# Kernel tuning notes

Hardware: AMD Instinct MI355X
Metric: run time of the kernel (lower is better)

Reference implementation:

```python
import jax, jax.numpy as jnp
import numpy as np
import math

PAD_IDX = 1
BOS_IDX = 2
B, S, T = 32, 128, 64
E, H, L, V = 256, 512, 2, 32000


def _lstm_cell(gates, c):
    # torch gate order: i, f, g, o
    i, f, g, o = jnp.split(gates, 4, axis=-1)
    c_new = jax.nn.sigmoid(f) * c + jax.nn.sigmoid(i) * jnp.tanh(g)
    h_new = jax.nn.sigmoid(o) * jnp.tanh(c_new)
    return h_new, c_new


def _run_lstm_layer(x_tbi, Wih, Whh, b, h0, c0):
    def step(carry, x_t):
        h, c = carry
        h2, c2 = _lstm_cell(x_t @ Wih + h @ Whh + b, c)
        return (h2, c2), h2
    (hT, cT), ys = jax.lax.scan(step, (h0, c0), x_tbi)
    return ys, hT, cT


def setup_inputs() -> dict:
    key = jax.random.key(0)
    ks = iter(jax.random.split(key, 40))
    def w(shape, s=0.05):
        return jax.random.normal(next(ks), shape, jnp.float32) * s
    inp = {
        'src_tokens': jax.random.randint(next(ks), (B, S), 0, V, dtype=jnp.int32),
        'tgt_tokens': jax.random.randint(next(ks), (B, T), 0, V, dtype=jnp.int32),
        'src_emb': w((V, E), 0.02),
        'tgt_emb': w((V, E), 0.02),
        'enc_Wih0': w((E, 4 * H)), 'enc_Whh0': w((H, 4 * H)), 'enc_b0': jnp.zeros((4 * H,), jnp.float32),
        'enc_Wih1': w((H, 4 * H)), 'enc_Whh1': w((H, 4 * H)), 'enc_b1': jnp.zeros((4 * H,), jnp.float32),
        'dec_Wih0': w((E + H, 4 * H)), 'dec_Whh0': w((H, 4 * H)), 'dec_b0': jnp.zeros((4 * H,), jnp.float32),
        'dec_Wih1': w((H, 4 * H)), 'dec_Whh1': w((H, 4 * H)), 'dec_b1': jnp.zeros((4 * H,), jnp.float32),
        'attn_W': w((2 * H, H)), 'attn_b': jnp.zeros((H,), jnp.float32),
        'v_w': w((H,)),
        'coal_w': w((L, 1), 0.5), 'coal_b': jnp.zeros((1,), jnp.float32),
        'out_W': w((2 * H + E, V)), 'out_b': jnp.zeros((V,), jnp.float32),
    }
    return inp


def reference(src_tokens, tgt_tokens, src_emb, tgt_emb,
              enc_Wih0, enc_Whh0, enc_b0, enc_Wih1, enc_Whh1, enc_b1,
              dec_Wih0, dec_Whh0, dec_b0, dec_Wih1, dec_Whh1, dec_b1,
              attn_W, attn_b, v_w, coal_w, coal_b, out_W, out_b):
    Bq = src_tokens.shape[0]
    sqrtE_src = np.float32(math.sqrt(src_emb.shape[1]))
    sqrtE_tgt = np.float32(math.sqrt(tgt_emb.shape[1]))

    # ---- Encoder (2-layer LSTM, batch_first; dropout=0 eval) ----
    x = (src_emb[src_tokens] * sqrtE_src).transpose(1, 0, 2)  # (S,B,E)
    z = jnp.zeros((Bq, H), jnp.float32)
    ys0, hA, cA = _run_lstm_layer(x, enc_Wih0, enc_Whh0, enc_b0, z, z)
    ys1, hB, cB = _run_lstm_layer(ys0, enc_Wih1, enc_Whh1, enc_b1, z, z)
    enc_out = ys1.transpose(1, 0, 2)          # (B,S,H)
    hidden = jnp.stack([hA, hB])              # (L,B,H)
    cell = jnp.stack([cA, cB])

    mask = src_tokens != PAD_IDX              # (B,S)
    Wq, We = attn_W[:H], attn_W[H:]
    enc_proj = enc_out @ We                   # (B,S,H) loop-invariant part of attn linear

    def dec_step(carry, tok):
        h, c = carry                          # (L,B,H) each
        emb = jax.nn.relu(tgt_emb[tok] * sqrtE_tgt)          # (B,E)
        # faithful raw reshape (L,B,H) -> (B,H,L), coalesce layers
        q = jax.nn.relu(h.reshape(Bq, H, L) @ coal_w + coal_b)[..., 0]  # (B,H)
        e = jnp.tanh(enc_proj + (q @ Wq + attn_b)[:, None, :])          # (B,S,H)
        score = e @ v_w                                                 # (B,S)
        score = jnp.where(mask, score, np.float32(-1e10))
        a = jax.nn.softmax(score, axis=1)
        wctx = jnp.einsum('bs,bsh->bh', a, enc_out)                     # (B,H)
        xin = jnp.concatenate([emb, wctx], axis=-1)                     # (B,E+H)
        h0n, c0n = _lstm_cell(xin @ dec_Wih0 + h[0] @ dec_Whh0 + dec_b0, c[0])
        h1n, c1n = _lstm_cell(h0n @ dec_Wih1 + h[1] @ dec_Whh1 + dec_b1, c[1])
        logits = jnp.concatenate([h1n, wctx, emb], axis=-1) @ out_W + out_b  # (B,V)
        return (jnp.stack([h0n, h1n]), jnp.stack([c0n, c1n])), logits

    (hF, cF), outs = jax.lax.scan(dec_step, (hidden, cell), tgt_tokens[:, :-1].T)
    first = jnp.full((Bq, 1, out_b.shape[0]), np.float32(BOS_IDX))  # decoder_outputs[:,0]=BOS_IDX
    dec_outputs = jnp.concatenate([first, outs.transpose(1, 0, 2)], axis=1)  # (B,T,V)
    return dec_outputs, hF, cF
```

## Files before the change

### kernel.cpp

```cpp
#include <hip/hip_runtime.h>
#include <hip/hip_bf16.h>

typedef __bf16 bf16x8 __attribute__((ext_vector_type(8)));
typedef float f32x4 __attribute__((ext_vector_type(4)));

#define DEV static __device__ __forceinline__

constexpr int Bq = 32, Sq = 128, Tq = 64, Eq = 256, Hq = 512, Vq = 32000;
constexpr int G4 = 2048;
constexpr int TD = 63;
constexpr int KOUT = 1280;
constexpr float SQRTE = 16.0f;

DEV float sigf(float x) { return 1.0f / (1.0f + __expf(-x)); }
DEV float tanh_fast(float x) {
    float ax = fabsf(x);
    float t = __expf(-2.f * ax);
    float r = (1.f - t) / (1.f + t);
    return x < 0.f ? -r : r;
}

__global__ __launch_bounds__(256) void k_embed_src(const int* __restrict__ tok,
                                                   const float* __restrict__ emb,
                                                   __hip_bfloat16* __restrict__ x)
{
    int idx = blockIdx.x * 256 + threadIdx.x;
    int e = idx & (Eq - 1);
    int r = idx >> 8;
    int b = r & 31, t = r >> 5;
    x[idx] = __float2bfloat16(emb[(size_t)tok[b * Sq + t] * Eq + e] * SQRTE);
}

__global__ __launch_bounds__(256) void k_embed_tgt(const int* __restrict__ tok,
                                                   const float* __restrict__ emb,
                                                   __hip_bfloat16* __restrict__ embt,
                                                   __hip_bfloat16* __restrict__ Xout)
{
    int idx = blockIdx.x * 256 + threadIdx.x;
    int e = idx & (Eq - 1);
    int r = idx >> 8;
    int b = r & 31, t = r >> 5;
    float v = fmaxf(0.f, emb[(size_t)tok[b * Tq + t] * Eq + e] * SQRTE);
    embt[idx] = __float2bfloat16(v);
    Xout[(size_t)r * KOUT + 1024 + e] = __float2bfloat16(v);
}

__global__ __launch_bounds__(256) void k_transpose_bf16(const float* __restrict__ W,
                                                        __hip_bfloat16* __restrict__ Wt,
                                                        int K, int N)
{
    __shared__ float tile[32][33];
    int nb = blockIdx.x * 32, kb = blockIdx.y * 32;
    int c = threadIdx.x & 31, r4 = threadIdx.x >> 5;
    for (int i = 0; i < 32; i += 8)
        tile[r4 + i][c] = W[(size_t)(kb + r4 + i) * N + nb + c];
    __syncthreads();
    for (int i = 0; i < 32; i += 8) {
        int rr = r4 + i;
        Wt[(size_t)(nb + rr) * K + kb + c] = __float2bfloat16(tile[c][rr]);
    }
}

DEV void stage_A(const __hip_bfloat16* A, __bf16* As) {
    int tx = threadIdx.x;
#pragma unroll
    for (int p = 0; p < 8; ++p) {
        int c = tx + p * 256;
        int row = c >> 6, kc = c & 63;
        uint4 v = *(const uint4*)((const unsigned short*)A + row * 512 + kc * 8);
        int kd = kc ^ (row & 7);
        *(uint4*)(As + row * 512 + kd * 8) = v;
    }
}

DEV void mfma_pass(const __bf16* As, const unsigned short* BT, int colB,
                   int kg, int fr, f32x4* acc) {
    const unsigned short* bp = BT + (size_t)colB * 512 + kg * 8;
    int f7 = fr & 7;
#pragma unroll
    for (int k0 = 0; k0 < 512; k0 += 32) {
        int cidx = ((k0 >> 3) | kg) ^ f7;
        bf16x8 bfv = *(const bf16x8*)(bp + k0);
        bf16x8 af0 = *(const bf16x8*)(As + fr * 512 + cidx * 8);
        bf16x8 af1 = *(const bf16x8*)(As + (16 + fr) * 512 + cidx * 8);
        acc[0] = __builtin_amdgcn_mfma_f32_16x16x32_bf16(af0, bfv, acc[0], 0, 0, 0);
        acc[1] = __builtin_amdgcn_mfma_f32_16x16x32_bf16(af1, bfv, acc[1], 0, 0, 0);
    }
}

DEV void rec_core(const __hip_bfloat16* A0, const __hip_bfloat16* B0T,
                  const __hip_bfloat16* A1, const __hip_bfloat16* B1T,
                  const __hip_bfloat16* xpart, const float* bias,
                  float* cbuf, float* hf, __hip_bfloat16* hb,
                  float* ef32, int ef32_stride,
                  __hip_bfloat16* ebf16, int ebf16_stride,
                  int j0, __bf16* As0, __bf16* As1)
{
    stage_A(A0, As0);
    if (A1) stage_A(A1, As1);
    __syncthreads();

    int tx = threadIdx.x, w = tx >> 6, lane = tx & 63;
    int fr = lane & 15, kg = lane >> 4;
    int colB = w * 512 + j0 + fr;

    f32x4 acc[2];
    acc[0] = (f32x4){0.f, 0.f, 0.f, 0.f};
    acc[1] = (f32x4){0.f, 0.f, 0.f, 0.f};
    mfma_pass(As0, (const unsigned short*)B0T, colB, kg, fr, acc);
    if (B1T) mfma_pass(As1, (const unsigned short*)B1T, colB, kg, fr, acc);

    __syncthreads();
    float* gbuf = (float*)As0;
    float* gw = gbuf + w * 512;
#pragma unroll
    for (int m = 0; m < 2; ++m)
#pragma unroll
        for (int q = 0; q < 4; ++q)
            gw[(m * 16 + kg * 4 + q) * 16 + fr] = acc[m][q];
    __syncthreads();

    int idx = tx;
#pragma unroll
    for (int r = 0; r < 2; ++r, idx += 256) {
        int b = idx >> 4, jj = idx & 15, j = j0 + jj;
        float gi = gbuf[0 * 512 + b * 16 + jj];
        float gf = gbuf[1 * 512 + b * 16 + jj];
        float gg = gbuf[2 * 512 + b * 16 + jj];
        float go = gbuf[3 * 512 + b * 16 + jj];
        if (xpart) {
            gi += __bfloat162float(xpart[b * 2048 + j]);
            gf += __bfloat162float(xpart[b * 2048 + 512 + j]);
            gg += __bfloat162float(xpart[b * 2048 + 1024 + j]);
            go += __bfloat162float(xpart[b * 2048 + 1536 + j]);
        }
        if (bias) {
            gi += bias[j]; gf += bias[512 + j];
            gg += bias[1024 + j]; go += bias[1536 + j];
        }
        int ci = b * 512 + j;
        float cc = cbuf[ci];
        float cn = sigf(gf) * cc + sigf(gi) * tanh_fast(gg);
        cbuf[ci] = cn;
        float ho = sigf(go) * tanh_fast(cn);
        hf[ci] = ho;
        hb[ci] = __float2bfloat16(ho);
        if (ef32)  ef32[b * ef32_stride + j] = ho;
        if (ebf16) ebf16[b * ebf16_stride + j] = __float2bfloat16(ho);
    }
}

__global__ __launch_bounds__(256) void k_rec(
    const __hip_bfloat16* __restrict__ A0, const __hip_bfloat16* __restrict__ B0T,
    const __hip_bfloat16* __restrict__ A1, const __hip_bfloat16* __restrict__ B1T,
    const __hip_bfloat16* __restrict__ xpart, const float* __restrict__ bias,
    float* __restrict__ cbuf, float* __restrict__ hf, __hip_bfloat16* __restrict__ hb,
    __hip_bfloat16* __restrict__ ebf16, int ebf16_stride)
{
    __shared__ __align__(16) __bf16 As0[32 * 512];
    __shared__ __align__(16) __bf16 As1[32 * 512];
    rec_core(A0, B0T, A1, B1T, xpart, bias, cbuf, hf, hb,
             nullptr, 0, ebf16, ebf16_stride, blockIdx.x * 16, As0, As1);
}

__global__ __launch_bounds__(256) void k_enc2(int t,
    const __hip_bfloat16* __restrict__ X0b,
    const __hip_bfloat16* __restrict__ eWhh0T, const __hip_bfloat16* __restrict__ eWih1T,
    const __hip_bfloat16* __restrict__ eWhh1T, const float* __restrict__ eb1,
    __hip_bfloat16* __restrict__ h0b, __hip_bfloat16* __restrict__ h1b,
    float* __restrict__ h0f, float* __restrict__ h1f,
    float* __restrict__ c0, float* __restrict__ c1,
    __hip_bfloat16* __restrict__ ys0b,
    float* __restrict__ encf, __hip_bfloat16* __restrict__ encb)
{
    __shared__ __align__(16) __bf16 As0[32 * 512];
    __shared__ __align__(16) __bf16 As1[32 * 512];
    bool lay1 = blockIdx.x >= 32;
    int j0 = (blockIdx.x & 31) * 16;
    if (!lay1) {
        if (t >= 128) return;
        rec_core(h0b + (t & 1) * 16384, eWhh0T, nullptr, nullptr,
                 X0b + (size_t)t * 32 * 2048, nullptr,
                 c0, h0f, h0b + ((t + 1) & 1) * 16384,
                 nullptr, 0, ys0b + (size_t)t * 16384, 512, j0, As0, As1);
    } else {
        if (t < 1) return;
        int s = t - 1;
        rec_core(ys0b + (size_t)s * 16384, eWih1T,
                 h1b + (s & 1) * 16384, eWhh1T,
                 nullptr, eb1,
                 c1, h1f, h1b + ((s + 1) & 1) * 16384,
                 encf + s * 512, 128 * 512, encb + s * 512, 128 * 512, j0, As0, As1);
    }
}

__global__ __launch_bounds__(256) void k_attnq(
    const float* __restrict__ h0f, const float* __restrict__ h1f,
    const __hip_bfloat16* __restrict__ WqT, const float* __restrict__ attn_b,
    const float* __restrict__ coal_w, const float* __restrict__ coal_b,
    float* __restrict__ aq)
{
    __shared__ __align__(16) __bf16 Qs[32 * 512];
    int tx = threadIdx.x;
    float cw0 = coal_w[0], cw1 = coal_w[1], cb = coal_b[0];
    for (int idx = tx; idx < 16384; idx += 256) {
        int b = idx >> 9, j = idx & 511;
        int p = b * 1024 + 2 * j;
        float v0 = (p < 16384) ? h0f[p] : h1f[p - 16384];
        float v1 = (p + 1 < 16384) ? h0f[p + 1] : h1f[p + 1 - 16384];
        float q = fmaxf(0.f, v0 * cw0 + v1 * cw1 + cb);
        int kc = j >> 3, kd = kc ^ (b & 7);
        Qs[b * 512 + kd * 8 + (j & 7)] = __float2bfloat16(q);
    }
    __syncthreads();
    int w = tx >> 6, lane = tx & 63, fr = lane & 15, kg = lane >> 4;
    int col = blockIdx.x * 64 + w * 16 + fr;
    f32x4 acc[2];
    acc[0] = (f32x4){0.f, 0.f, 0.f, 0.f};
    acc[1] = (f32x4){0.f, 0.f, 0.f, 0.f};
    mfma_pass(Qs, (const unsigned short*)WqT, col, kg, fr, acc);
    float ab = attn_b[col];
#pragma unroll
    for (int m = 0; m < 2; ++m)
#pragma unroll
        for (int q = 0; q < 4; ++q)
            aq[(m * 16 + kg * 4 + q) * 512 + col] = acc[m][q] + ab;
}

__global__ __launch_bounds__(256) void k_attnsc(
    const float* __restrict__ aq, const float* __restrict__ v_w,
    const int* __restrict__ src_tok,
    const float* __restrict__ enc_proj, const float* __restrict__ enc_outf,
    __hip_bfloat16* __restrict__ wctxb, __hip_bfloat16* __restrict__ XoutT)
{
    __shared__ float aqs[512];
    __shared__ float vws[512];
    __shared__ float sc[128];
    int b = blockIdx.x;
    int tx = threadIdx.x;
    for (int i = tx; i < 512; i += 256) { aqs[i] = aq[b * 512 + i]; vws[i] = v_w[i]; }
    __syncthreads();

    int s = tx >> 1, half = tx & 1;
    const float* ep = enc_proj + ((size_t)(b * 128 + s)) * 512 + half * 256;
    float a0 = 0.f, a1 = 0.f, a2 = 0.f, a3 = 0.f;
#pragma unroll 8
    for (int ii = 0; ii < 256; ii += 4) {
        float4 f = *(const float4*)(ep + ii);
        int ib = half * 256 + ii;
        a0 += tanh_fast(f.x + aqs[ib])     * vws[ib];
        a1 += tanh_fast(f.y + aqs[ib + 1]) * vws[ib + 1];
        a2 += tanh_fast(f.z + aqs[ib + 2]) * vws[ib + 2];
        a3 += tanh_fast(f.w + aqs[ib + 3]) * vws[ib + 3];
    }
    float p = (a0 + a1) + (a2 + a3);
    p += __shfl_xor(p, 1, 64);
    if (half == 0) sc[s] = (src_tok[b * 128 + s] != 1) ? p : -1e10f;
    __syncthreads();

    if (tx < 64) {
        float m1 = fmaxf(sc[tx], sc[tx + 64]);
#pragma unroll
        for (int o = 32; o > 0; o >>= 1) m1 = fmaxf(m1, __shfl_down(m1, o, 64));
        m1 = __shfl(m1, 0, 64);
        float e0 = __expf(sc[tx] - m1), e1 = __expf(sc[tx + 64] - m1);
        float ss = e0 + e1;
#pragma unroll
        for (int o = 32; o > 0; o >>= 1) ss += __shfl_down(ss, o, 64);
        ss = __shfl(ss, 0, 64);
        float inv = 1.0f / ss;
        sc[tx] = e0 * inv; sc[tx + 64] = e1 * inv;
    }
    __syncthreads();

#pragma unroll
    for (int rr = 0; rr < 2; ++rr) {
        int i = tx + rr * 256;
        const float* eo = enc_outf + (size_t)b * 65536 + i;
        float w0 = 0.f, w1 = 0.f, w2 = 0.f, w3 = 0.f;
#pragma unroll 8
        for (int s2 = 0; s2 < 128; s2 += 4) {
            w0 += sc[s2]     * eo[(s2)     * 512];
            w1 += sc[s2 + 1] * eo[(s2 + 1) * 512];
            w2 += sc[s2 + 2] * eo[(s2 + 2) * 512];
            w3 += sc[s2 + 3] * eo[(s2 + 3) * 512];
        }
        float wv = (w0 + w1) + (w2 + w3);
        wctxb[b * 512 + i] = __float2bfloat16(wv);
        XoutT[(size_t)b * KOUT + 512 + i] = __float2bfloat16(wv);
    }
}

__global__ __launch_bounds__(256) void k_mfma(
    const __hip_bfloat16* __restrict__ A, const __hip_bfloat16* __restrict__ BT,
    const float* __restrict__ bias, float* __restrict__ Cf,
    __hip_bfloat16* __restrict__ Cb, int M, int N, int K)
{
    __shared__ __bf16 As[128][72];
    __shared__ __bf16 Bs[128][72];
    const unsigned short* Aw = (const unsigned short*)A;
    const unsigned short* Bw = (const unsigned short*)BT;
    int n0 = blockIdx.x * 128, m0 = blockIdx.y * 128;
    int tx = threadIdx.x;
    int w = tx >> 6, lane = tx & 63;
    int wm = (w >> 1) * 64, wn = (w & 1) * 64;
    int fr = lane & 15, kg = lane >> 4;
    f32x4 acc[4][4];
#pragma unroll
    for (int mi = 0; mi < 4; mi++)
#pragma unroll
        for (int ni = 0; ni < 4; ni++) acc[mi][ni] = (f32x4){0.f, 0.f, 0.f, 0.f};

    for (int k0 = 0; k0 < K; k0 += 64) {
        __syncthreads();
#pragma unroll
        for (int p = 0; p < 4; p++) {
            int ch = tx + p * 256;
            int r = ch >> 3, cc = (ch & 7) * 8;
            uint4 va = {0u, 0u, 0u, 0u};
            int m = m0 + r;
            if (m < M) va = *(const uint4*)(Aw + (size_t)m * K + k0 + cc);
            *(uint4*)(&As[r][cc]) = va;
            uint4 vb = *(const uint4*)(Bw + (size_t)(n0 + r) * K + k0 + cc);
            *(uint4*)(&Bs[r][cc]) = vb;
        }
        __syncthreads();
#pragma unroll
        for (int kk = 0; kk < 64; kk += 32) {
            bf16x8 af[4], bfv[4];
#pragma unroll
            for (int i = 0; i < 4; i++) {
                af[i]  = *(const bf16x8*)(&As[wm + i * 16 + fr][kk + kg * 8]);
                bfv[i] = *(const bf16x8*)(&Bs[wn + i * 16 + fr][kk + kg * 8]);
            }
#pragma unroll
            for (int mi = 0; mi < 4; mi++)
#pragma unroll
                for (int ni = 0; ni < 4; ni++)
                    acc[mi][ni] = __builtin_amdgcn_mfma_f32_16x16x32_bf16(
                        af[mi], bfv[ni], acc[mi][ni], 0, 0, 0);
        }
    }
#pragma unroll
    for (int ni = 0; ni < 4; ni++) {
        int n = n0 + wn + ni * 16 + fr;
        float bv = bias ? bias[n] : 0.f;
#pragma unroll
        for (int mi = 0; mi < 4; mi++) {
#pragma unroll
            for (int qd = 0; qd < 4; qd++) {
                int R = m0 + wm + mi * 16 + kg * 4 + qd;
                if (R < M) {
                    float v = acc[mi][ni][qd] + bv;
                    if (Cf) Cf[(size_t)R * N + n] = v;
                    else    Cb[(size_t)R * N + n] = __float2bfloat16(v);
                }
            }
        }
    }
}

__global__ __launch_bounds__(256) void k_init_dec(
    const float* __restrict__ h0e, const float* __restrict__ h1e,
    const float* __restrict__ c0e, const float* __restrict__ c1e,
    float* __restrict__ h0fd, float* __restrict__ h1fd,
    __hip_bfloat16* __restrict__ h0bd, __hip_bfloat16* __restrict__ h1bd,
    float* __restrict__ c0d, float* __restrict__ c1d)
{
    int idx = blockIdx.x * 256 + threadIdx.x;
    float a = h0e[idx], b = h1e[idx];
    h0fd[idx] = a; h1fd[idx] = b;
    h0bd[idx] = __float2bfloat16(a);
    h1bd[idx] = __float2bfloat16(b);
    c0d[idx] = c0e[idx];
    c1d[idx] = c1e[idx];
}

__global__ __launch_bounds__(256) void k_bos(float* __restrict__ out)
{
    int b = blockIdx.y;
    int i = blockIdx.x * 256 + threadIdx.x;
    out[(size_t)b * (Tq * Vq) + i] = 2.0f;
}

__global__ __launch_bounds__(256) void k_finalize(
    const float* __restrict__ h0f, const float* __restrict__ h1f,
    const float* __restrict__ c0f, const float* __restrict__ c1f,
    float* __restrict__ out)
{
    int idx = blockIdx.x * 256 + threadIdx.x;
    size_t base = (size_t)Bq * Tq * Vq;
    out[base + idx] = h0f[idx];
    out[base + 16384 + idx] = h1f[idx];
    out[base + 32768 + idx] = c0f[idx];
    out[base + 49152 + idx] = c1f[idx];
}

__global__ __launch_bounds__(256) void k_logits(
    const __hip_bfloat16* __restrict__ A, const __hip_bfloat16* __restrict__ Bt,
    const float* __restrict__ bias, float* __restrict__ out)
{
    __shared__ __bf16 As[128][72];
    __shared__ __bf16 Bs[128][72];
    const unsigned short* Aw = (const unsigned short*)A;
    const unsigned short* Bw = (const unsigned short*)Bt;
    int n0 = blockIdx.x * 128, m0 = blockIdx.y * 128;
    int tx = threadIdx.x;
    int w = tx >> 6, lane = tx & 63;
    int wm = (w >> 1) * 64, wn = (w & 1) * 64;
    int fr = lane & 15, kg = lane >> 4;
    f32x4 acc[4][4];
#pragma unroll
    for (int mi = 0; mi < 4; mi++)
#pragma unroll
        for (int ni = 0; ni < 4; ni++) acc[mi][ni] = (f32x4){0.f, 0.f, 0.f, 0.f};

    for (int k0 = 0; k0 < 1280; k0 += 64) {
        __syncthreads();
#pragma unroll
        for (int p = 0; p < 4; p++) {
            int ch = tx + p * 256;
            int r = ch >> 3, cc = (ch & 7) * 8;
            uint4 va = {0u, 0u, 0u, 0u};
            int m = m0 + r;
            if (m < 2016) va = *(const uint4*)(Aw + (size_t)m * 1280 + k0 + cc);
            *(uint4*)(&As[r][cc]) = va;
            uint4 vb = *(const uint4*)(Bw + (size_t)(n0 + r) * 1280 + k0 + cc);
            *(uint4*)(&Bs[r][cc]) = vb;
        }
        __syncthreads();
#pragma unroll
        for (int kk = 0; kk < 64; kk += 32) {
            bf16x8 af[4], bfv[4];
#pragma unroll
            for (int i = 0; i < 4; i++) {
                af[i]  = *(const bf16x8*)(&As[wm + i * 16 + fr][kk + kg * 8]);
                bfv[i] = *(const bf16x8*)(&Bs[wn + i * 16 + fr][kk + kg * 8]);
            }
#pragma unroll
            for (int mi = 0; mi < 4; mi++)
#pragma unroll
                for (int ni = 0; ni < 4; ni++)
                    acc[mi][ni] = __builtin_amdgcn_mfma_f32_16x16x32_bf16(
                        af[mi], bfv[ni], acc[mi][ni], 0, 0, 0);
        }
    }
#pragma unroll
    for (int ni = 0; ni < 4; ni++) {
        int n = n0 + wn + ni * 16 + fr;
        float bv = bias[n];
#pragma unroll
        for (int mi = 0; mi < 4; mi++) {
#pragma unroll
            for (int qd = 0; qd < 4; qd++) {
                int R = m0 + wm + mi * 16 + kg * 4 + qd;
                if (R < 2016) {
                    int bb = R & 31, ts = R >> 5;
                    out[(size_t)bb * (Tq * Vq) + (size_t)(ts + 1) * Vq + n] =
                        acc[mi][ni][qd] + bv;
                }
            }
        }
    }
}

extern "C" void kernel_launch(void* const* d_in, const int* in_sizes, int n_in,
                              void* d_out, int out_size, void* d_ws, size_t ws_size,
                              hipStream_t stream)
{
    (void)in_sizes; (void)n_in; (void)out_size; (void)ws_size;
    const int*   src_tok = (const int*)  d_in[0];
    const int*   tgt_tok = (const int*)  d_in[1];
    const float* src_emb = (const float*)d_in[2];
    const float* tgt_emb = (const float*)d_in[3];
    const float* eWih0   = (const float*)d_in[4];
    const float* eWhh0   = (const float*)d_in[5];
    const float* eb0     = (const float*)d_in[6];
    const float* eWih1   = (const float*)d_in[7];
    const float* eWhh1   = (const float*)d_in[8];
    const float* eb1     = (const float*)d_in[9];
    const float* dWih0   = (const float*)d_in[10];
    const float* dWhh0   = (const float*)d_in[11];
    const float* db0     = (const float*)d_in[12];
    const float* dWih1   = (const float*)d_in[13];
    const float* dWhh1   = (const float*)d_in[14];
    const float* db1     = (const float*)d_in[15];
    const float* attn_W  = (const float*)d_in[16];
    const float* attn_b  = (const float*)d_in[17];
    const float* v_w     = (const float*)d_in[18];
    const float* coal_w  = (const float*)d_in[19];
    const float* coal_b  = (const float*)d_in[20];
    const float* out_W   = (const float*)d_in[21];
    const float* out_b   = (const float*)d_in[22];
    float* out = (float*)d_out;

    char* ws = (char*)d_ws;
    size_t off = 0;
    auto alloc = [&](size_t bytes) -> char* {
        char* p = ws + off;
        off += (bytes + 255) & ~(size_t)255;
        return p;
    };
    typedef __hip_bfloat16 BF;
    BF* X0b     = (BF*)alloc(4096ull * 2048 * 2);
    BF* Xembb   = (BF*)alloc(2016ull * 2048 * 2);
    BF* x_srcb  = (BF*)alloc(4096ull * 256 * 2);
    BF* embtb   = (BF*)alloc(2016ull * 256 * 2);
    BF* ys0b    = (BF*)alloc(128ull * 16384 * 2);
    float* enc_outf = (float*)alloc(4096ull * 512 * 4);
    BF* enc_outb    = (BF*)alloc(4096ull * 512 * 2);
    float* enc_proj = (float*)alloc(4096ull * 512 * 4);
    float* aq       = (float*)alloc(16384ull * 4);
    BF* wctxb       = (BF*)alloc(16384ull * 2);
    BF* Xout        = (BF*)alloc(2016ull * 1280 * 2);
    BF* Wt          = (BF*)alloc(32000ull * 1280 * 2);
    BF* eWhh0T  = (BF*)alloc(2048ull * 512 * 2);
    BF* eWih1T  = (BF*)alloc(2048ull * 512 * 2);
    BF* eWhh1T  = (BF*)alloc(2048ull * 512 * 2);
    BF* dWih0wT = (BF*)alloc(2048ull * 512 * 2);
    BF* dWhh0T  = (BF*)alloc(2048ull * 512 * 2);
    BF* dWih1T  = (BF*)alloc(2048ull * 512 * 2);
    BF* dWhh1T  = (BF*)alloc(2048ull * 512 * 2);
    BF* eWih0T  = (BF*)alloc(2048ull * 256 * 2);
    BF* dWih0eT = (BF*)alloc(2048ull * 256 * 2);
    BF* WqT     = (BF*)alloc(512ull * 512 * 2);
    BF* WeT     = (BF*)alloc(512ull * 512 * 2);
    BF* h0b_e   = (BF*)alloc(2ull * 16384 * 2);
    BF* h1b_e   = (BF*)alloc(2ull * 16384 * 2);
    float* h0f_e = (float*)alloc(16384ull * 4);
    float* h1f_e = (float*)alloc(16384ull * 4);
    float* c0e   = (float*)alloc(16384ull * 4);
    float* c1e   = (float*)alloc(16384ull * 4);
    float* h0fd  = (float*)alloc(2ull * 16384 * 4);
    float* h1fd  = (float*)alloc(2ull * 16384 * 4);
    BF* h0bd     = (BF*)alloc(2ull * 16384 * 2);
    BF* h1bd     = (BF*)alloc(2ull * 16384 * 2);
    float* c0d   = (float*)alloc(16384ull * 4);
    float* c1d   = (float*)alloc(16384ull * 4);

    hipMemsetAsync(h0b_e, 0, 2 * 16384 * 2, stream);
    hipMemsetAsync(h1b_e, 0, 2 * 16384 * 2, stream);
    hipMemsetAsync(c0e, 0, 16384 * 4, stream);
    hipMemsetAsync(c1e, 0, 16384 * 4, stream);

    k_embed_src<<<4096, 256, 0, stream>>>(src_tok, src_emb, x_srcb);
    k_embed_tgt<<<2016, 256, 0, stream>>>(tgt_tok, tgt_emb, embtb, Xout);

    k_transpose_bf16<<<dim3(64, 16), 256, 0, stream>>>(eWhh0, eWhh0T, 512, 2048);
    k_transpose_bf16<<<dim3(64, 16), 256, 0, stream>>>(eWih1, eWih1T, 512, 2048);
    k_transpose_bf16<<<dim3(64, 16), 256, 0, stream>>>(eWhh1, eWhh1T, 512, 2048);
    k_transpose_bf16<<<dim3(64, 16), 256, 0, stream>>>(dWih0 + 256 * 2048, dWih0wT, 512, 2048);
    k_transpose_bf16<<<dim3(64, 16), 256, 0, stream>>>(dWhh0, dWhh0T, 512, 2048);
    k_transpose_bf16<<<dim3(64, 16), 256, 0, stream>>>(dWih1, dWih1T, 512, 2048);
    k_transpose_bf16<<<dim3(64, 16), 256, 0, stream>>>(dWhh1, dWhh1T, 512, 2048);
    k_transpose_bf16<<<dim3(64, 8), 256, 0, stream>>>(eWih0, eWih0T, 256, 2048);
    k_transpose_bf16<<<dim3(64, 8), 256, 0, stream>>>(dWih0, dWih0eT, 256, 2048);
    k_transpose_bf16<<<dim3(16, 16), 256, 0, stream>>>(attn_W, WqT, 512, 512);
    k_transpose_bf16<<<dim3(16, 16), 256, 0, stream>>>(attn_W + 512 * 512, WeT, 512, 512);
    k_transpose_bf16<<<dim3(1000, 40), 256, 0, stream>>>(out_W, Wt, 1280, 32000);

    k_mfma<<<dim3(16, 32), 256, 0, stream>>>(x_srcb, eWih0T, eb0, nullptr, X0b, 4096, 2048, 256);
    k_mfma<<<dim3(16, 16), 256, 0, stream>>>(embtb, dWih0eT, db0, nullptr, Xembb, 2016, 2048, 256);
    k_bos<<<dim3(125, 32), 256, 0, stream>>>(out);

    for (int t = 0; t <= 128; ++t)
        k_enc2<<<64, 256, 0, stream>>>(t, X0b, eWhh0T, eWih1T, eWhh1T, eb1,
                                       h0b_e, h1b_e, h0f_e, h1f_e, c0e, c1e,
                                       ys0b, enc_outf, enc_outb);

    k_mfma<<<dim3(4, 32), 256, 0, stream>>>(enc_outb, WeT, nullptr, enc_proj, nullptr, 4096, 512, 512);

    k_init_dec<<<64, 256, 0, stream>>>(h0f_e, h1f_e, c0e, c1e,
                                       h0fd, h1fd, h0bd, h1bd, c0d, c1d);

    for (int t = 0; t < TD; ++t) {
        int cur = t & 1, nxt = (t + 1) & 1;
        BF* XoutT = Xout + (size_t)t * 32 * KOUT;
        k_attnq<<<8, 256, 0, stream>>>(h0fd + cur * 16384, h1fd + cur * 16384,
                                       WqT, attn_b, coal_w, coal_b, aq);
        k_attnsc<<<32, 256, 0, stream>>>(aq, v_w, src_tok, enc_proj, enc_outf,
                                         wctxb, XoutT);
        k_rec<<<32, 256, 0, stream>>>(wctxb, dWih0wT,
                                      h0bd + cur * 16384, dWhh0T,
                                      Xembb + (size_t)t * 32 * 2048, nullptr,
                                      c0d, h0fd + nxt * 16384, h0bd + nxt * 16384,
                                      nullptr, 0);
        k_rec<<<32, 256, 0, stream>>>(h0bd + nxt * 16384, dWih1T,
                                      h1bd + cur * 16384, dWhh1T,
                                      nullptr, db1,
                                      c1d, h1fd + nxt * 16384, h1bd + nxt * 16384,
                                      XoutT, KOUT);
    }
    k_finalize<<<64, 256, 0, stream>>>(h0fd + (TD & 1) * 16384, h1fd + (TD & 1) * 16384,
                                       c0d, c1d, out);
    k_logits<<<dim3(250, 16), 256, 0, stream>>>(Xout, Wt, out_b, out);
}
```

Baseline: 4.791 ms.

## Replace per-step encoder and decoder launches with persistent kernels and grid barriers

The encoder's 129 launches and the decoder's 4×63 launches are replaced by two persistent 64-block kernels that step through time and synchronise with a software grid barrier built on atomics. The decoder attention is also reorganised: 64 blocks each take half the source positions and emit unnormalised partial contexts plus exp sums. These are combined and normalised inside the layer-0 recurrence step, which skips the max subtraction and uses a clamped tanh. This removes launch overhead and inter-kernel gaps, at the cost of spin-wait barriers that depend on all 64 blocks being co-resident and a softmax without max subtraction.

```diff
diff --git a/kernel.cpp b/kernel.cpp
--- a/kernel.cpp
+++ b/kernel.cpp
@@ -18,6 +18,32 @@
     float t = __expf(-2.f * ax);
     float r = (1.f - t) / (1.f + t);
     return x < 0.f ? -r : r;
+}
+DEV float tanh_c(float x) {
+    float xc = fminf(fmaxf(x, -15.f), 15.f);
+    float t = __expf(2.f * xc);
+    return (t - 1.f) / (t + 1.f);
+}
+
+DEV void gbar(unsigned* cnt, unsigned* gen, unsigned nblk) {
+    __syncthreads();
+    if (threadIdx.x == 0) {
+        __threadfence();
+        unsigned g = __hip_atomic_load(gen, __ATOMIC_RELAXED, __HIP_MEMORY_SCOPE_AGENT);
+        unsigned old = __hip_atomic_fetch_add(cnt, 1u, __ATOMIC_ACQ_REL, __HIP_MEMORY_SCOPE_AGENT);
+        if (old == nblk - 1u) {
+            __hip_atomic_store(cnt, 0u, __ATOMIC_RELAXED, __HIP_MEMORY_SCOPE_AGENT);
+            __hip_atomic_fetch_add(gen, 1u, __ATOMIC_ACQ_REL, __HIP_MEMORY_SCOPE_AGENT);
+        } else {
+            unsigned cg;
+            do {
+                __builtin_amdgcn_s_sleep(2);
+                cg = __hip_atomic_load(gen, __ATOMIC_ACQUIRE, __HIP_MEMORY_SCOPE_AGENT);
+            } while (cg == g);
+        }
+        __threadfence();
+    }
+    __syncthreads();
 }
 
 __global__ __launch_bounds__(256) void k_embed_src(const int* __restrict__ tok,
@@ -88,18 +114,12 @@
     }
 }
 
-DEV void rec_core(const __hip_bfloat16* A0, const __hip_bfloat16* B0T,
-                  const __hip_bfloat16* A1, const __hip_bfloat16* B1T,
-                  const __hip_bfloat16* xpart, const float* bias,
-                  float* cbuf, float* hf, __hip_bfloat16* hb,
-                  float* ef32, int ef32_stride,
-                  __hip_bfloat16* ebf16, int ebf16_stride,
-                  int j0, __bf16* As0, __bf16* As1)
-{
-    stage_A(A0, As0);
-    if (A1) stage_A(A1, As1);
-    __syncthreads();
-
+DEV void rec_compute(const __hip_bfloat16* B0T, const __hip_bfloat16* B1T,
+                     const __hip_bfloat16* xpart, const float* bias,
+                     float* cbuf, float* hf, __hip_bfloat16* hb,
+                     float* ef32, int ef32s, __hip_bfloat16* ebf16, int ebs,
+                     int j0, __bf16* As0, __bf16* As1)
+{
     int tx = threadIdx.x, w = tx >> 6, lane = tx & 63;
     int fr = lane & 15, kg = lane >> 4;
     int colB = w * 512 + j0 + fr;
@@ -145,25 +165,26 @@
         float ho = sigf(go) * tanh_fast(cn);
         hf[ci] = ho;
         hb[ci] = __float2bfloat16(ho);
-        if (ef32)  ef32[b * ef32_stride + j] = ho;
-        if (ebf16) ebf16[b * ebf16_stride + j] = __float2bfloat16(ho);
-    }
-}
-
-__global__ __launch_bounds__(256) void k_rec(
-    const __hip_bfloat16* __restrict__ A0, const __hip_bfloat16* __restrict__ B0T,
-    const __hip_bfloat16* __restrict__ A1, const __hip_bfloat16* __restrict__ B1T,
-    const __hip_bfloat16* __restrict__ xpart, const float* __restrict__ bias,
-    float* __restrict__ cbuf, float* __restrict__ hf, __hip_bfloat16* __restrict__ hb,
-    __hip_bfloat16* __restrict__ ebf16, int ebf16_stride)
-{
-    __shared__ __align__(16) __bf16 As0[32 * 512];
-    __shared__ __align__(16) __bf16 As1[32 * 512];
-    rec_core(A0, B0T, A1, B1T, xpart, bias, cbuf, hf, hb,
-             nullptr, 0, ebf16, ebf16_stride, blockIdx.x * 16, As0, As1);
-}
-
-__global__ __launch_bounds__(256) void k_enc2(int t,
+        if (ef32)  ef32[b * ef32s + j] = ho;
+        if (ebf16) ebf16[b * ebs + j] = __float2bfloat16(ho);
+    }
+}
+
+DEV void rec_core(const __hip_bfloat16* A0, const __hip_bfloat16* B0T,
+                  const __hip_bfloat16* A1, const __hip_bfloat16* B1T,
+                  const __hip_bfloat16* xpart, const float* bias,
+                  float* cbuf, float* hf, __hip_bfloat16* hb,
+                  float* ef32, int ef32s, __hip_bfloat16* ebf16, int ebs,
+                  int j0, __bf16* As0, __bf16* As1)
+{
+    stage_A(A0, As0);
+    if (A1) stage_A(A1, As1);
+    __syncthreads();
+    rec_compute(B0T, B1T, xpart, bias, cbuf, hf, hb,
+                ef32, ef32s, ebf16, ebs, j0, As0, As1);
+}
+
+__global__ __launch_bounds__(256) void k_enc_persist(
     const __hip_bfloat16* __restrict__ X0b,
     const __hip_bfloat16* __restrict__ eWhh0T, const __hip_bfloat16* __restrict__ eWih1T,
     const __hip_bfloat16* __restrict__ eWhh1T, const float* __restrict__ eb1,
@@ -171,123 +192,172 @@
     float* __restrict__ h0f, float* __restrict__ h1f,
     float* __restrict__ c0, float* __restrict__ c1,
     __hip_bfloat16* __restrict__ ys0b,
-    float* __restrict__ encf, __hip_bfloat16* __restrict__ encb)
+    float* __restrict__ encf, __hip_bfloat16* __restrict__ encb,
+    unsigned* __restrict__ gb)
 {
     __shared__ __align__(16) __bf16 As0[32 * 512];
     __shared__ __align__(16) __bf16 As1[32 * 512];
     bool lay1 = blockIdx.x >= 32;
     int j0 = (blockIdx.x & 31) * 16;
-    if (!lay1) {
-        if (t >= 128) return;
-        rec_core(h0b + (t & 1) * 16384, eWhh0T, nullptr, nullptr,
-                 X0b + (size_t)t * 32 * 2048, nullptr,
-                 c0, h0f, h0b + ((t + 1) & 1) * 16384,
-                 nullptr, 0, ys0b + (size_t)t * 16384, 512, j0, As0, As1);
-    } else {
-        if (t < 1) return;
-        int s = t - 1;
-        rec_core(ys0b + (size_t)s * 16384, eWih1T,
-                 h1b + (s & 1) * 16384, eWhh1T,
-                 nullptr, eb1,
-                 c1, h1f, h1b + ((s + 1) & 1) * 16384,
-                 encf + s * 512, 128 * 512, encb + s * 512, 128 * 512, j0, As0, As1);
-    }
-}
-
-__global__ __launch_bounds__(256) void k_attnq(
-    const float* __restrict__ h0f, const float* __restrict__ h1f,
+    unsigned* cnt = gb;
+    unsigned* gen = gb + 16;
+    for (int t = 0; t <= 128; ++t) {
+        if (!lay1) {
+            if (t < 128)
+                rec_core(h0b + (t & 1) * 16384, eWhh0T, nullptr, nullptr,
+                         X0b + (size_t)t * 32 * 2048, nullptr,
+                         c0, h0f, h0b + ((t + 1) & 1) * 16384,
+                         nullptr, 0, ys0b + (size_t)t * 16384, 512, j0, As0, As1);
+        } else {
+            if (t >= 1) {
+                int s = t - 1;
+                rec_core(ys0b + (size_t)s * 16384, eWih1T,
+                         h1b + (s & 1) * 16384, eWhh1T,
+                         nullptr, eb1,
+                         c1, h1f, h1b + ((s + 1) & 1) * 16384,
+                         encf + s * 512, 128 * 512, encb + s * 512, 128 * 512,
+                         j0, As0, As1);
+            }
+        }
+        gbar(cnt, gen, 64);
+    }
+}
+
+__global__ __launch_bounds__(256) void k_dec_persist(
+    const float* __restrict__ enc_proj, const float* __restrict__ enc_outf,
+    const int* __restrict__ src_tok, const float* __restrict__ v_w,
     const __hip_bfloat16* __restrict__ WqT, const float* __restrict__ attn_b,
     const float* __restrict__ coal_w, const float* __restrict__ coal_b,
-    float* __restrict__ aq)
-{
-    __shared__ __align__(16) __bf16 Qs[32 * 512];
-    int tx = threadIdx.x;
-    float cw0 = coal_w[0], cw1 = coal_w[1], cb = coal_b[0];
-    for (int idx = tx; idx < 16384; idx += 256) {
-        int b = idx >> 9, j = idx & 511;
-        int p = b * 1024 + 2 * j;
-        float v0 = (p < 16384) ? h0f[p] : h1f[p - 16384];
-        float v1 = (p + 1 < 16384) ? h0f[p + 1] : h1f[p + 1 - 16384];
-        float q = fmaxf(0.f, v0 * cw0 + v1 * cw1 + cb);
-        int kc = j >> 3, kd = kc ^ (b & 7);
-        Qs[b * 512 + kd * 8 + (j & 7)] = __float2bfloat16(q);
-    }
-    __syncthreads();
-    int w = tx >> 6, lane = tx & 63, fr = lane & 15, kg = lane >> 4;
-    int col = blockIdx.x * 64 + w * 16 + fr;
-    f32x4 acc[2];
-    acc[0] = (f32x4){0.f, 0.f, 0.f, 0.f};
-    acc[1] = (f32x4){0.f, 0.f, 0.f, 0.f};
-    mfma_pass(Qs, (const unsigned short*)WqT, col, kg, fr, acc);
-    float ab = attn_b[col];
-#pragma unroll
-    for (int m = 0; m < 2; ++m)
-#pragma unroll
-        for (int q = 0; q < 4; ++q)
-            aq[(m * 16 + kg * 4 + q) * 512 + col] = acc[m][q] + ab;
-}
-
-__global__ __launch_bounds__(256) void k_attnsc(
-    const float* __restrict__ aq, const float* __restrict__ v_w,
-    const int* __restrict__ src_tok,
-    const float* __restrict__ enc_proj, const float* __restrict__ enc_outf,
-    __hip_bfloat16* __restrict__ wctxb, __hip_bfloat16* __restrict__ XoutT)
-{
-    __shared__ float aqs[512];
-    __shared__ float vws[512];
-    __shared__ float sc[128];
-    int b = blockIdx.x;
-    int tx = threadIdx.x;
-    for (int i = tx; i < 512; i += 256) { aqs[i] = aq[b * 512 + i]; vws[i] = v_w[i]; }
-    __syncthreads();
-
-    int s = tx >> 1, half = tx & 1;
-    const float* ep = enc_proj + ((size_t)(b * 128 + s)) * 512 + half * 256;
-    float a0 = 0.f, a1 = 0.f, a2 = 0.f, a3 = 0.f;
+    const __hip_bfloat16* __restrict__ dWih0wT, const __hip_bfloat16* __restrict__ dWhh0T,
+    const __hip_bfloat16* __restrict__ dWih1T, const __hip_bfloat16* __restrict__ dWhh1T,
+    const float* __restrict__ db1, const __hip_bfloat16* __restrict__ Xembb,
+    float* __restrict__ h0fd, float* __restrict__ h1fd,
+    __hip_bfloat16* __restrict__ h0bd, __hip_bfloat16* __restrict__ h1bd,
+    float* __restrict__ c0d, float* __restrict__ c1d,
+    float* __restrict__ aq, float* __restrict__ pctx, float* __restrict__ psum,
+    __hip_bfloat16* __restrict__ Xout,
+    unsigned* __restrict__ gb)
+{
+    __shared__ __align__(16) __bf16 As0[32 * 512];
+    __shared__ __align__(16) __bf16 As1[32 * 512];
+    __shared__ float rsum[32];
+    int bid = blockIdx.x, tx = threadIdx.x;
+    unsigned* cnt = gb + 32;
+    unsigned* gen = gb + 48;
+
+    for (int t = 0; t < TD; ++t) {
+        int cur = t & 1, nxt = cur ^ 1;
+        const float* h0c = h0fd + cur * 16384;
+        const float* h1c = h1fd + cur * 16384;
+        __hip_bfloat16* XoutT = Xout + (size_t)t * 32 * KOUT;
+
+        if (bid < 8) {
+            __bf16* Qs = As0;
+            float cw0 = coal_w[0], cw1 = coal_w[1], cb = coal_b[0];
+            for (int idx = tx; idx < 16384; idx += 256) {
+                int b2 = idx >> 9, j = idx & 511;
+                int p = b2 * 1024 + 2 * j;
+                float v0 = (p < 16384) ? h0c[p] : h1c[p - 16384];
+                float v1 = (p + 1 < 16384) ? h0c[p + 1] : h1c[p + 1 - 16384];
+                float q = fmaxf(0.f, v0 * cw0 + v1 * cw1 + cb);
+                int kc = j >> 3, kd = kc ^ (b2 & 7);
+                Qs[b2 * 512 + kd * 8 + (j & 7)] = __float2bfloat16(q);
+            }
+            __syncthreads();
+            int w = tx >> 6, lane = tx & 63, fr = lane & 15, kg = lane >> 4;
+            int col = bid * 64 + w * 16 + fr;
+            f32x4 acc[2];
+            acc[0] = (f32x4){0.f, 0.f, 0.f, 0.f};
+            acc[1] = (f32x4){0.f, 0.f, 0.f, 0.f};
+            mfma_pass(Qs, (const unsigned short*)WqT, col, kg, fr, acc);
+            float ab = attn_b[col];
+#pragma unroll
+            for (int m = 0; m < 2; ++m)
+#pragma unroll
+                for (int q = 0; q < 4; ++q)
+                    aq[(m * 16 + kg * 4 + q) * 512 + col] = acc[m][q] + ab;
+        }
+        gbar(cnt, gen, 64);
+
+        {
+            int b = bid & 31, half = bid >> 5;
+            float* aqs = (float*)As0;
+            float* vws = aqs + 512;
+            float* ws  = vws + 512;
+            for (int i = tx; i < 512; i += 256) {
+                aqs[i] = aq[b * 512 + i];
+                vws[i] = v_w[i];
+            }
+            __syncthreads();
+            int sl = tx >> 2, lq = tx & 3;
+            int s = half * 64 + sl;
+            const float* ep = enc_proj + ((size_t)(b * 128 + s)) * 512 + lq * 128;
+            float a0 = 0.f, a1 = 0.f, a2 = 0.f, a3 = 0.f;
 #pragma unroll 8
-    for (int ii = 0; ii < 256; ii += 4) {
-        float4 f = *(const float4*)(ep + ii);
-        int ib = half * 256 + ii;
-        a0 += tanh_fast(f.x + aqs[ib])     * vws[ib];
-        a1 += tanh_fast(f.y + aqs[ib + 1]) * vws[ib + 1];
-        a2 += tanh_fast(f.z + aqs[ib + 2]) * vws[ib + 2];
-        a3 += tanh_fast(f.w + aqs[ib + 3]) * vws[ib + 3];
-    }
-    float p = (a0 + a1) + (a2 + a3);
-    p += __shfl_xor(p, 1, 64);
-    if (half == 0) sc[s] = (src_tok[b * 128 + s] != 1) ? p : -1e10f;
-    __syncthreads();
-
-    if (tx < 64) {
-        float m1 = fmaxf(sc[tx], sc[tx + 64]);
-#pragma unroll
-        for (int o = 32; o > 0; o >>= 1) m1 = fmaxf(m1, __shfl_down(m1, o, 64));
-        m1 = __shfl(m1, 0, 64);
-        float e0 = __expf(sc[tx] - m1), e1 = __expf(sc[tx + 64] - m1);
-        float ss = e0 + e1;
-#pragma unroll
-        for (int o = 32; o > 0; o >>= 1) ss += __shfl_down(ss, o, 64);
-        ss = __shfl(ss, 0, 64);
-        float inv = 1.0f / ss;
-        sc[tx] = e0 * inv; sc[tx + 64] = e1 * inv;
-    }
-    __syncthreads();
-
-#pragma unroll
-    for (int rr = 0; rr < 2; ++rr) {
-        int i = tx + rr * 256;
-        const float* eo = enc_outf + (size_t)b * 65536 + i;
-        float w0 = 0.f, w1 = 0.f, w2 = 0.f, w3 = 0.f;
-#pragma unroll 8
-        for (int s2 = 0; s2 < 128; s2 += 4) {
-            w0 += sc[s2]     * eo[(s2)     * 512];
-            w1 += sc[s2 + 1] * eo[(s2 + 1) * 512];
-            w2 += sc[s2 + 2] * eo[(s2 + 2) * 512];
-            w3 += sc[s2 + 3] * eo[(s2 + 3) * 512];
-        }
-        float wv = (w0 + w1) + (w2 + w3);
-        wctxb[b * 512 + i] = __float2bfloat16(wv);
-        XoutT[(size_t)b * KOUT + 512 + i] = __float2bfloat16(wv);
+            for (int ii = 0; ii < 128; ii += 4) {
+                float4 f = *(const float4*)(ep + ii);
+                int ib = lq * 128 + ii;
+                a0 += tanh_c(f.x + aqs[ib])     * vws[ib];
+                a1 += tanh_c(f.y + aqs[ib + 1]) * vws[ib + 1];
+                a2 += tanh_c(f.z + aqs[ib + 2]) * vws[ib + 2];
+                a3 += tanh_c(f.w + aqs[ib + 3]) * vws[ib + 3];
+            }
+            float p = (a0 + a1) + (a2 + a3);
+            p += __shfl_xor(p, 1, 64);
+            p += __shfl_xor(p, 2, 64);
+            if (lq == 0)
+                ws[sl] = (src_tok[b * 128 + s] != 1) ? __expf(p) : 0.f;
+            __syncthreads();
+            float acc0 = 0.f, acc1 = 0.f;
+            const float* eo = enc_outf + ((size_t)b * 128 + half * 64) * 512;
+#pragma unroll 4
+            for (int s2 = 0; s2 < 64; ++s2) {
+                float wv = ws[s2];
+                acc0 += wv * eo[(size_t)s2 * 512 + tx];
+                acc1 += wv * eo[(size_t)s2 * 512 + tx + 256];
+            }
+            pctx[(size_t)(b * 2 + half) * 512 + tx] = acc0;
+            pctx[(size_t)(b * 2 + half) * 512 + tx + 256] = acc1;
+            if (tx < 64) {
+                float ss = ws[tx];
+#pragma unroll
+                for (int o = 32; o > 0; o >>= 1) ss += __shfl_down(ss, o, 64);
+                if (tx == 0) psum[b * 2 + half] = ss;
+            }
+        }
+        gbar(cnt, gen, 64);
+
+        if (bid < 32) {
+            int j0 = bid * 16;
+            if (tx < 32) rsum[tx] = 1.0f / (psum[tx * 2] + psum[tx * 2 + 1]);
+            __syncthreads();
+            for (int idx = tx; idx < 16384; idx += 256) {
+                int b2 = idx >> 9, i = idx & 511;
+                float wv = (pctx[(size_t)(b2 * 2) * 512 + i] +
+                            pctx[(size_t)(b2 * 2 + 1) * 512 + i]) * rsum[b2];
+                int kc = i >> 3, kd = kc ^ (b2 & 7);
+                As0[b2 * 512 + kd * 8 + (i & 7)] = __float2bfloat16(wv);
+                if (bid == 0)
+                    XoutT[(size_t)b2 * KOUT + 512 + i] = __float2bfloat16(wv);
+            }
+            stage_A(h0bd + cur * 16384, As1);
+            __syncthreads();
+            rec_compute(dWih0wT, dWhh0T,
+                        Xembb + (size_t)t * 32 * 2048, nullptr,
+                        c0d, h0fd + nxt * 16384, h0bd + nxt * 16384,
+                        nullptr, 0, nullptr, 0, j0, As0, As1);
+        }
+        gbar(cnt, gen, 64);
+
+        if (bid < 32) {
+            int j0 = bid * 16;
+            rec_core(h0bd + nxt * 16384, dWih1T,
+                     h1bd + cur * 16384, dWhh1T,
+                     nullptr, db1,
+                     c1d, h1fd + nxt * 16384, h1bd + nxt * 16384,
+                     nullptr, 0, XoutT, KOUT, j0, As0, As1);
+        }
+        gbar(cnt, gen, 64);
     }
 }
 
@@ -511,7 +581,8 @@
     BF* enc_outb    = (BF*)alloc(4096ull * 512 * 2);
     float* enc_proj = (float*)alloc(4096ull * 512 * 4);
     float* aq       = (float*)alloc(16384ull * 4);
-    BF* wctxb       = (BF*)alloc(16384ull * 2);
+    float* pctx     = (float*)alloc(64ull * 512 * 4);
+    float* psum     = (float*)alloc(64ull * 4);
     BF* Xout        = (BF*)alloc(2016ull * 1280 * 2);
     BF* Wt          = (BF*)alloc(32000ull * 1280 * 2);
     BF* eWhh0T  = (BF*)alloc(2048ull * 512 * 2);
@@ -537,7 +608,9 @@
     BF* h1bd     = (BF*)alloc(2ull * 16384 * 2);
     float* c0d   = (float*)alloc(16384ull * 4);
     float* c1d   = (float*)alloc(16384ull * 4);
-
+    unsigned* gbb = (unsigned*)alloc(256);
+
+    hipMemsetAsync(gbb, 0, 256, stream);
     hipMemsetAsync(h0b_e, 0, 2 * 16384 * 2, stream);
     hipMemsetAsync(h1b_e, 0, 2 * 16384 * 2, stream);
     hipMemsetAsync(c0e, 0, 16384 * 4, stream);
@@ -563,34 +636,22 @@
     k_mfma<<<dim3(16, 16), 256, 0, stream>>>(embtb, dWih0eT, db0, nullptr, Xembb, 2016, 2048, 256);
     k_bos<<<dim3(125, 32), 256, 0, stream>>>(out);
 
-    for (int t = 0; t <= 128; ++t)
-        k_enc2<<<64, 256, 0, stream>>>(t, X0b, eWhh0T, eWih1T, eWhh1T, eb1,
-                                       h0b_e, h1b_e, h0f_e, h1f_e, c0e, c1e,
-                                       ys0b, enc_outf, enc_outb);
+    k_enc_persist<<<64, 256, 0, stream>>>(X0b, eWhh0T, eWih1T, eWhh1T, eb1,
+                                          h0b_e, h1b_e, h0f_e, h1f_e, c0e, c1e,
+                                          ys0b, enc_outf, enc_outb, gbb);
 
     k_mfma<<<dim3(4, 32), 256, 0, stream>>>(enc_outb, WeT, nullptr, enc_proj, nullptr, 4096, 512, 512);
 
     k_init_dec<<<64, 256, 0, stream>>>(h0f_e, h1f_e, c0e, c1e,
                                        h0fd, h1fd, h0bd, h1bd, c0d, c1d);
 
-    for (int t = 0; t < TD; ++t) {
-        int cur = t & 1, nxt = (t + 1) & 1;
-        BF* XoutT = Xout + (size_t)t * 32 * KOUT;
-        k_attnq<<<8, 256, 0, stream>>>(h0fd + cur * 16384, h1fd + cur * 16384,
-                                       WqT, attn_b, coal_w, coal_b, aq);
-        k_attnsc<<<32, 256, 0, stream>>>(aq, v_w, src_tok, enc_proj, enc_outf,
-                                         wctxb, XoutT);
-        k_rec<<<32, 256, 0, stream>>>(wctxb, dWih0wT,
-                                      h0bd + cur * 16384, dWhh0T,
-                                      Xembb + (size_t)t * 32 * 2048, nullptr,
-                                      c0d, h0fd + nxt * 16384, h0bd + nxt * 16384,
-                                      nullptr, 0);
-        k_rec<<<32, 256, 0, stream>>>(h0bd + nxt * 16384, dWih1T,
-                                      h1bd + cur * 16384, dWhh1T,
-                                      nullptr, db1,
-                                      c1d, h1fd + nxt * 16384, h1bd + nxt * 16384,
-                                      XoutT, KOUT);
-    }
+    k_dec_persist<<<64, 256, 0, stream>>>(enc_proj, enc_outf, src_tok, v_w,
+                                          WqT, attn_b, coal_w, coal_b,
+                                          dWih0wT, dWhh0T, dWih1T, dWhh1T,
+                                          db1, Xembb,
+                                          h0fd, h1fd, h0bd, h1bd, c0d, c1d,
+                                          aq, pctx, psum, Xout, gbb);
+
     k_finalize<<<64, 256, 0, stream>>>(h0fd + (TD & 1) * 16384, h1fd + (TD & 1) * 16384,
                                        c0d, c1d, out);
     k_logits<<<dim3(250, 16), 256, 0, stream>>>(Xout, Wt, out_b, out);
```

Result: slower. 7.911 ms (+65.1%).
